# Kernel optimization log

Hardware: AMD Instinct MI355X
Metric: run time of the kernel (lower is better)

Reference implementation:

```python
import jax, jax.numpy as jnp
import numpy as np

EMBED_DIMS = 256

def setup_inputs() -> dict:
    key = jax.random.key(0)
    ks = jax.random.split(key, 6)
    C = EMBED_DIMS
    x = jax.random.normal(ks[0], (4, 2048, C), dtype=jnp.float32)
    prev_x = jax.random.normal(ks[1], (4, 2048, C), dtype=jnp.float32)
    s = 1.0 / np.sqrt(C)
    W_qkv = jax.random.uniform(ks[2], (C, 3 * C), dtype=jnp.float32, minval=-s, maxval=s)
    b_qkv = jax.random.uniform(ks[3], (3 * C,), dtype=jnp.float32, minval=-s, maxval=s)
    W_out = jax.random.uniform(ks[4], (C, C), dtype=jnp.float32, minval=-s, maxval=s)
    b_out = jax.random.uniform(ks[5], (C,), dtype=jnp.float32, minval=-s, maxval=s)
    return {"x": x, "prev_x": prev_x, "W_qkv": W_qkv, "b_qkv": b_qkv,
            "W_out": W_out, "b_out": b_out}

def reference(x, prev_x, W_qkv, b_qkv, W_out, b_out):
    B, N, C = x.shape
    xx = jnp.concatenate([prev_x, x], axis=1)          # [B, S, C], S = 2N
    qkv = xx @ W_qkv + b_qkv                            # [B, S, 3C]
    q, k, v = jnp.split(qkv, 3, axis=-1)                # each [B, S, C]
    scale = 1.0 / jnp.sqrt(jnp.asarray(C, dtype=x.dtype))
    attn = jax.nn.softmax(jnp.einsum('bqc,bkc->bqk', q, k) * scale, axis=-1)
    out = jnp.einsum('bqk,bkc->bqc', attn, v)           # [B, S, C]
    out = out @ W_out + b_out
    return out[:, -N:, :]                               # [B, N, C]
```

## Files before the change

### kernel.cpp

```cpp
#include <hip/hip_runtime.h>

typedef __bf16 bf16;
typedef __attribute__((ext_vector_type(8))) __bf16 bf16x8;
typedef __attribute__((ext_vector_type(4))) __bf16 bf16x4;
typedef __attribute__((ext_vector_type(4))) float f32x4;
typedef __attribute__((ext_vector_type(16))) float f32x16;
typedef __attribute__((ext_vector_type(4))) unsigned u32x4;

#define MFMA16(a, b, c) __builtin_amdgcn_mfma_f32_16x16x32_bf16(a, b, c, 0, 0, 0)
#define MFMA32(a, b, c) __builtin_amdgcn_mfma_f32_32x32x16_bf16(a, b, c, 0, 0, 0)

__device__ inline void gload_lds16(const void* g, void* l) {
  __builtin_amdgcn_global_load_lds(
      (const __attribute__((address_space(1))) void*)g,
      (__attribute__((address_space(3))) void*)l, 16, 0, 0);
}

__device__ inline unsigned packbf(float a, float b) {
  unsigned short x = __builtin_bit_cast(unsigned short, (bf16)a);
  unsigned short y = __builtin_bit_cast(unsigned short, (bf16)b);
  return (unsigned)x | ((unsigned)y << 16);
}

__global__ __launch_bounds__(256) void prep_w_kernel(
    const float* __restrict__ Wqkv, const float* __restrict__ Wout,
    bf16* __restrict__ Wqkvt, bf16* __restrict__ Woutt)
{
  int tid = blockIdx.x * 256 + threadIdx.x;
  int nth = gridDim.x * 256;
  for (int i = tid; i < 768 * 256; i += nth) {
    int n = i >> 8, k = i & 255;
    Wqkvt[i] = (bf16)Wqkv[k * 768 + n];
  }
  for (int i = tid; i < 256 * 256; i += nth) {
    int n = i >> 8, k = i & 255;
    Woutt[i] = (bf16)Wout[k * 256 + n];
  }
}

__global__ __launch_bounds__(256) void gemm_qkv_kernel(
    const float* __restrict__ x, const float* __restrict__ px,
    const bf16* __restrict__ Wt, const float* __restrict__ bias,
    bf16* __restrict__ Qo, bf16* __restrict__ KVo)
{
  const int bm = blockIdx.x * 64;
  const int n0 = blockIdx.y * 128;
  const int tid = threadIdx.x;
  const int lane = tid & 63, w = tid >> 6;
  const int l15 = lane & 15, lg = lane >> 4;

  alignas(16) __shared__ bf16 Alds[64 * 32];
  alignas(16) __shared__ bf16 Wlds[128 * 32];

  f32x4 acc[8] = {};

  for (int k0 = 0; k0 < 256; k0 += 32) {
    __syncthreads();
    {
      int c = tid;
      int row = c >> 2, kc = (c & 3) << 3;
      const int m = bm + row;
      const int b = m >> 12;
      const int s = m & 4095;
      const float* src = (s < 2048)
          ? (px + ((size_t)b << 19) + (size_t)s * 256 + k0 + kc)
          : (x + ((size_t)b << 19) + (size_t)(s - 2048) * 256 + k0 + kc);
      float4 f0 = *(const float4*)src;
      float4 f1 = *(const float4*)(src + 4);
      bf16x8 v = { (bf16)f0.x, (bf16)f0.y, (bf16)f0.z, (bf16)f0.w,
                   (bf16)f1.x, (bf16)f1.y, (bf16)f1.z, (bf16)f1.w };
      *(bf16x8*)((char*)Alds + ((c << 4) ^ (((row >> 1) & 3) << 4))) = v;
    }
    #pragma unroll
    for (int it = 0; it < 2; it++) {
      int c = it * 256 + tid;
      int row = c >> 2, kc = (c & 3) << 3;
      bf16x8 v = *(const bf16x8*)(Wt + (size_t)(n0 + row) * 256 + k0 + kc);
      *(bf16x8*)((char*)Wlds + ((c << 4) ^ (((row >> 1) & 3) << 4))) = v;
    }
    __syncthreads();
    const int arow = w * 16 + l15;
    bf16x8 afr = *(const bf16x8*)((char*)Alds +
        (((arow << 6) + (lg << 4)) ^ (((arow >> 1) & 3) << 4)));
    #pragma unroll
    for (int nt = 0; nt < 8; nt++) {
      const int wrow = nt * 16 + l15;
      bf16x8 bfr = *(const bf16x8*)((char*)Wlds +
          (((wrow << 6) + (lg << 4)) ^ (((wrow >> 1) & 3) << 4)));
      acc[nt] = MFMA16(afr, bfr, acc[nt]);
    }
  }

  #pragma unroll
  for (int nt = 0; nt < 8; nt++) {
    const int n = n0 + nt * 16 + l15;
    const float bv = bias[n];
    const int m0 = bm + w * 16 + lg * 4;
    const int bq = m0 >> 12;
    const int s = m0 & 4095;
    if (n < 256) {
      if (s >= 2048) {
        const int ks = n >> 4, h2 = (n >> 3) & 1, e = n & 7;
        #pragma unroll
        for (int r = 0; r < 4; r++) {
          const int qrow = bq * 2048 + (s - 2048) + r;
          Qo[(size_t)(qrow >> 5) * 8192 + ks * 512 +
             ((qrow & 31) + 32 * h2) * 8 + e] =
              (bf16)((acc[nt][r] + bv) * 0.0625f);
        }
      }
    } else if (n < 512) {
      const int d = n - 256;
      const int ks = d >> 4, h2 = (d >> 3) & 1, e = d & 7;
      const size_t tb = (size_t)(bq * 128 + (s >> 5)) * 16384;
      #pragma unroll
      for (int r = 0; r < 4; r++)
        KVo[tb + ks * 512 + (((s & 31) + r) + 32 * h2) * 8 + e] =
            (bf16)(acc[nt][r] + bv);
    } else {
      const int d = n - 512;
      const int kv32 = s & 31;
      const int sidx = kv32 >> 4, h2 = (kv32 >> 3) & 1, e0 = kv32 & 7;
      bf16x4 st = { (bf16)(acc[nt][0] + bv), (bf16)(acc[nt][1] + bv),
                    (bf16)(acc[nt][2] + bv), (bf16)(acc[nt][3] + bv) };
      *(bf16x4*)(KVo + (size_t)(bq * 128 + (s >> 5)) * 16384 + 8192 +
                 (sidx * 8 + (d >> 5)) * 512 + ((d & 31) + 32 * h2) * 8 + e0) = st;
    }
  }
}

__global__ __launch_bounds__(256, 2) void attn_kernel(
    const bf16* __restrict__ Qp, const bf16* __restrict__ KVp,
    bf16* __restrict__ Opart, float* __restrict__ ml)
{
  const int id = blockIdx.x;
  const int c = id & 7;
  const int b = (id >> 3) & 3;
  const int qb = id >> 5;
  const int tid = threadIdx.x;
  const int lane = tid & 63, w = tid >> 6;
  const int l31 = lane & 31, hi = lane >> 5;

  __shared__ bf16 lds[2][16384];

  const int qg = b * 64 + qb * 4 + w;
  const bf16* qbase = Qp + (size_t)qg * 8192 + lane * 8;
  bf16x8 qf[16];
  #pragma unroll
  for (int ks = 0; ks < 16; ks++)
    qf[ks] = *(const bf16x8*)(qbase + ks * 512);

  const bf16* kvtile0 = KVp + (size_t)(b * 128 + c * 16) * 16384;

  auto stage = [&](int t) {
    const char* g = (const char*)(kvtile0 + (size_t)t * 16384) + w * 8192 + lane * 16;
    char* l = (char*)&lds[t & 1][0] + w * 8192;
    #pragma unroll
    for (int j = 0; j < 8; j++)
      gload_lds16(g + j * 1024, l + j * 1024);
  };
  stage(0);

  f32x16 o[8] = {};
  float m_run = -1e30f, l_run = 0.f;

  for (int t = 0; t < 16; t++) {
    __syncthreads();
    if (t + 1 < 16) stage(t + 1);
    const bf16* kbuf = &lds[t & 1][0];
    const bf16* vbuf = kbuf + 8192;

    f32x16 p = {};
    __builtin_amdgcn_s_setprio(1);
    #pragma unroll
    for (int ks = 0; ks < 16; ks++) {
      bf16x8 kf = *(const bf16x8*)(kbuf + ks * 512 + lane * 8);
      p = MFMA32(kf, qf[ks], p);
    }
    __builtin_amdgcn_s_setprio(0);

    float mt = fmaxf(p[0], p[1]);
    #pragma unroll
    for (int i = 2; i < 16; i++) mt = fmaxf(mt, p[i]);
    mt = fmaxf(mt, __shfl_xor(mt, 32));
    if (!__all(mt <= m_run + 8.f)) {
      const float m_new = fmaxf(m_run, mt);
      const float alpha = __expf(m_run - m_new);
      l_run *= alpha;
      #pragma unroll
      for (int i = 0; i < 8; i++)
        #pragma unroll
        for (int j = 0; j < 16; j++) o[i][j] *= alpha;
      m_run = m_new;
    }
    float ps = 0.f;
    #pragma unroll
    for (int i = 0; i < 16; i++) { p[i] = __expf(p[i] - m_run); ps += p[i]; }
    ps += __shfl_xor(ps, 32);
    l_run += ps;

    unsigned u[8], xp[8];
    #pragma unroll
    for (int i = 0; i < 8; i++) u[i] = packbf(p[2 * i], p[2 * i + 1]);
    #pragma unroll
    for (int i = 0; i < 8; i++)
      xp[i] = (unsigned)__shfl_xor((int)u[i], 32);
    const u32x4 w0 = hi ? (u32x4){xp[2], xp[3], u[2], u[3]}
                        : (u32x4){u[0], u[1], xp[0], xp[1]};
    const u32x4 w1 = hi ? (u32x4){xp[6], xp[7], u[6], u[7]}
                        : (u32x4){u[4], u[5], xp[4], xp[5]};
    const bf16x8 pf0 = __builtin_bit_cast(bf16x8, w0);
    const bf16x8 pf1 = __builtin_bit_cast(bf16x8, w1);

    __builtin_amdgcn_s_setprio(1);
    #pragma unroll
    for (int dg = 0; dg < 8; dg++) {
      bf16x8 v0 = *(const bf16x8*)(vbuf + dg * 512 + lane * 8);
      o[dg] = MFMA32(v0, pf0, o[dg]);
      bf16x8 v1 = *(const bf16x8*)(vbuf + (8 + dg) * 512 + lane * 8);
      o[dg] = MFMA32(v1, pf1, o[dg]);
    }
    __builtin_amdgcn_s_setprio(0);
  }

  const int q = b * 2048 + qb * 128 + w * 32 + l31;
  bf16* ob = Opart + ((size_t)c * 8192 + q) * 256;
  #pragma unroll
  for (int dg = 0; dg < 8; dg++) {
    #pragma unroll
    for (int r4 = 0; r4 < 4; r4++) {
      const int d = dg * 32 + r4 * 8 + hi * 4;
      bf16x4 st = { (bf16)o[dg][r4 * 4 + 0], (bf16)o[dg][r4 * 4 + 1],
                    (bf16)o[dg][r4 * 4 + 2], (bf16)o[dg][r4 * 4 + 3] };
      *(bf16x4*)(ob + d) = st;
    }
  }
  if (hi == 0) {
    float2 v = { m_run, l_run };
    *(float2*)(ml + ((size_t)c * 8192 + q) * 2) = v;
  }
}

__global__ __launch_bounds__(256) void out_kernel(
    const bf16* __restrict__ Opart, const float* __restrict__ ml,
    const bf16* __restrict__ Woutt, const float* __restrict__ bout,
    float* __restrict__ out)
{
  const int bm = blockIdx.x * 32;
  const int tid = threadIdx.x;
  const int lane = tid & 63, w = tid >> 6;
  const int l15 = lane & 15, lg = lane >> 4;

  alignas(16) __shared__ bf16 Alds[32 * 256];
  alignas(16) __shared__ bf16 Wlds[256 * 32];

  #pragma unroll
  for (int ch = 0; ch < 4; ch++) {
    const int idx = ch * 256 + tid;
    const int row = idx >> 5;
    const int dc = (idx & 31) << 3;
    const int q = bm + row;
    float ms[8], ls[8], M = -1e30f;
    #pragma unroll
    for (int s = 0; s < 8; s++) {
      float2 v = *(const float2*)(ml + ((size_t)s * 8192 + q) * 2);
      ms[s] = v.x; ls[s] = v.y;
      M = fmaxf(M, v.x);
    }
    float L = 0.f, acc[8] = {};
    #pragma unroll
    for (int s = 0; s < 8; s++) {
      const float wgt = __expf(ms[s] - M);
      L += ls[s] * wgt;
      bf16x8 v = *(const bf16x8*)(Opart + ((size_t)s * 8192 + q) * 256 + dc);
      #pragma unroll
      for (int j = 0; j < 8; j++) acc[j] += wgt * (float)v[j];
    }
    const float inv = 1.f / L;
    bf16x8 st;
    #pragma unroll
    for (int j = 0; j < 8; j++) st[j] = (bf16)(acc[j] * inv);
    *(bf16x8*)((char*)Alds + ((row * 512 + dc * 2) ^ ((row & 7) << 4))) = st;
  }

  f32x4 acc[8] = {};
  for (int k0 = 0; k0 < 8; k0++) {
    __syncthreads();
    #pragma unroll
    for (int it = 0; it < 4; it++) {
      int cidx = it * 256 + tid;
      int row = cidx >> 2, kc = (cidx & 3) << 3;
      bf16x8 v = *(const bf16x8*)(Woutt + (size_t)row * 256 + k0 * 32 + kc);
      *(bf16x8*)((char*)Wlds + ((cidx << 4) ^ (((row >> 1) & 3) << 4))) = v;
    }
    __syncthreads();
    const int arow = (w & 1) * 16 + l15;
    bf16x8 afr = *(const bf16x8*)((char*)Alds +
        ((arow * 512 + k0 * 64 + lg * 16) ^ ((arow & 7) << 4)));
    #pragma unroll
    for (int nt = 0; nt < 8; nt++) {
      const int wrow = (w >> 1) * 128 + nt * 16 + l15;
      bf16x8 bfr = *(const bf16x8*)((char*)Wlds +
          (((wrow << 6) + (lg << 4)) ^ (((wrow >> 1) & 3) << 4)));
      acc[nt] = MFMA16(afr, bfr, acc[nt]);
    }
  }

  #pragma unroll
  for (int nt = 0; nt < 8; nt++) {
    const int n = (w >> 1) * 128 + nt * 16 + l15;
    const float bvv = bout[n];
    const int m0 = bm + (w & 1) * 16 + lg * 4;
    #pragma unroll
    for (int r = 0; r < 4; r++)
      out[(size_t)(m0 + r) * 256 + n] = acc[nt][r] + bvv;
  }
}

extern "C" void kernel_launch(void* const* d_in, const int* in_sizes, int n_in,
                              void* d_out, int out_size, void* d_ws, size_t ws_size,
                              hipStream_t stream) {
  const float* x    = (const float*)d_in[0];
  const float* px   = (const float*)d_in[1];
  const float* Wqkv = (const float*)d_in[2];
  const float* bqkv = (const float*)d_in[3];
  const float* Wout = (const float*)d_in[4];
  const float* bout = (const float*)d_in[5];
  float* out = (float*)d_out;

  char* ws = (char*)d_ws;
  bf16* Qp    = (bf16*)(ws);
  bf16* KVp   = (bf16*)(ws + 4194304);
  bf16* Woutt = (bf16*)(ws + 20971520);
  bf16* Wqkvt = (bf16*)(ws + 21102592);
  float* ml   = (float*)(ws + 21495808);
  bf16* Opart = (bf16*)(ws + 22020096);

  prep_w_kernel<<<dim3(128), dim3(256), 0, stream>>>(Wqkv, Wout, Wqkvt, Woutt);
  gemm_qkv_kernel<<<dim3(256, 6), dim3(256), 0, stream>>>(
      x, px, Wqkvt, bqkv, Qp, KVp);
  attn_kernel<<<dim3(512), dim3(256), 0, stream>>>(Qp, KVp, Opart, ml);
  out_kernel<<<dim3(256), dim3(256), 0, stream>>>(Opart, ml, Woutt, bout, out);
}
```

Baseline: 93.51 us.

## Skip unused Q projection for prev rows, widen QKV tiles, async-stage weights

The QKV GEMM moves to a 1D grid that leaves out the Q column blocks for prev_x rows, whose queries are discarded anyway, and doubles the M tile to 128 rows so each wave runs two MFMA row tiles. Weight tiles in both GEMMs are now loaded straight into LDS with global_load_lds, with the swizzle applied to the source address. The output projection double-buffers the weight tile, prefetching the next K slice while the current one computes, which drops one barrier per iteration. The costs are more accumulator registers and reliance on the barrier to complete the async LDS loads.

```diff
diff --git a/kernel.cpp b/kernel.cpp
--- a/kernel.cpp
+++ b/kernel.cpp
@@ -43,28 +43,34 @@
     const bf16* __restrict__ Wt, const float* __restrict__ bias,
     bf16* __restrict__ Qo, bf16* __restrict__ KVo)
 {
-  const int bm = blockIdx.x * 64;
-  const int n0 = blockIdx.y * 128;
+  const int idb = blockIdx.x;
+  const int b = idb / 160;
+  const int r = idb % 160;
+  int mblk, y;
+  if (r < 64) { mblk = r >> 2; y = 2 + (r & 3); }
+  else { int r2 = r - 64; mblk = 16 + r2 / 6; y = r2 % 6; }
+  const int bm = b * 4096 + mblk * 128;
+  const int n0 = y * 128;
+
   const int tid = threadIdx.x;
   const int lane = tid & 63, w = tid >> 6;
   const int l15 = lane & 15, lg = lane >> 4;
 
-  alignas(16) __shared__ bf16 Alds[64 * 32];
+  alignas(16) __shared__ bf16 Alds[128 * 32];
   alignas(16) __shared__ bf16 Wlds[128 * 32];
 
-  f32x4 acc[8] = {};
+  f32x4 acc[2][8] = {};
+
+  const float* xsrc = ((bm & 4095) < 2048) ? px : x;
+  const size_t xbase = ((size_t)b << 19) + (size_t)(bm & 2047) * 256;
 
   for (int k0 = 0; k0 < 256; k0 += 32) {
     __syncthreads();
-    {
-      int c = tid;
+    #pragma unroll
+    for (int it = 0; it < 2; it++) {
+      int c = it * 256 + tid;
       int row = c >> 2, kc = (c & 3) << 3;
-      const int m = bm + row;
-      const int b = m >> 12;
-      const int s = m & 4095;
-      const float* src = (s < 2048)
-          ? (px + ((size_t)b << 19) + (size_t)s * 256 + k0 + kc)
-          : (x + ((size_t)b << 19) + (size_t)(s - 2048) * 256 + k0 + kc);
+      const float* src = xsrc + xbase + (size_t)row * 256 + k0 + kc;
       float4 f0 = *(const float4*)src;
       float4 f1 = *(const float4*)(src + 4);
       bf16x8 v = { (bf16)f0.x, (bf16)f0.y, (bf16)f0.z, (bf16)f0.w,
@@ -72,59 +78,68 @@
       *(bf16x8*)((char*)Alds + ((c << 4) ^ (((row >> 1) & 3) << 4))) = v;
     }
     #pragma unroll
-    for (int it = 0; it < 2; it++) {
-      int c = it * 256 + tid;
-      int row = c >> 2, kc = (c & 3) << 3;
-      bf16x8 v = *(const bf16x8*)(Wt + (size_t)(n0 + row) * 256 + k0 + kc);
-      *(bf16x8*)((char*)Wlds + ((c << 4) ^ (((row >> 1) & 3) << 4))) = v;
+    for (int jj = 0; jj < 2; jj++) {
+      int j = w * 2 + jj;
+      int row = j * 16 + (lane >> 2);
+      int chunk = (lane & 3) ^ ((row >> 1) & 3);
+      const bf16* g = Wt + (size_t)(n0 + row) * 256 + k0 + chunk * 8;
+      gload_lds16(g, (char*)Wlds + j * 1024);
     }
     __syncthreads();
-    const int arow = w * 16 + l15;
-    bf16x8 afr = *(const bf16x8*)((char*)Alds +
-        (((arow << 6) + (lg << 4)) ^ (((arow >> 1) & 3) << 4)));
+
+    const int arow0 = w * 32 + l15;
+    bf16x8 af0 = *(const bf16x8*)((char*)Alds +
+        (((arow0 << 6) + (lg << 4)) ^ (((arow0 >> 1) & 3) << 4)));
+    const int arow1 = arow0 + 16;
+    bf16x8 af1 = *(const bf16x8*)((char*)Alds +
+        (((arow1 << 6) + (lg << 4)) ^ (((arow1 >> 1) & 3) << 4)));
     #pragma unroll
     for (int nt = 0; nt < 8; nt++) {
       const int wrow = nt * 16 + l15;
       bf16x8 bfr = *(const bf16x8*)((char*)Wlds +
           (((wrow << 6) + (lg << 4)) ^ (((wrow >> 1) & 3) << 4)));
-      acc[nt] = MFMA16(afr, bfr, acc[nt]);
-    }
-  }
-
-  #pragma unroll
-  for (int nt = 0; nt < 8; nt++) {
-    const int n = n0 + nt * 16 + l15;
-    const float bv = bias[n];
-    const int m0 = bm + w * 16 + lg * 4;
-    const int bq = m0 >> 12;
-    const int s = m0 & 4095;
-    if (n < 256) {
-      if (s >= 2048) {
-        const int ks = n >> 4, h2 = (n >> 3) & 1, e = n & 7;
+      acc[0][nt] = MFMA16(af0, bfr, acc[0][nt]);
+      acc[1][nt] = MFMA16(af1, bfr, acc[1][nt]);
+    }
+  }
+
+  #pragma unroll
+  for (int mt = 0; mt < 2; mt++) {
+    #pragma unroll
+    for (int nt = 0; nt < 8; nt++) {
+      const int n = n0 + nt * 16 + l15;
+      const float bv = bias[n];
+      const int m0 = bm + w * 32 + mt * 16 + lg * 4;
+      const int bq = m0 >> 12;
+      const int s = m0 & 4095;
+      if (n < 256) {
+        if (s >= 2048) {
+          const int ks = n >> 4, h2 = (n >> 3) & 1, e = n & 7;
+          #pragma unroll
+          for (int rr = 0; rr < 4; rr++) {
+            const int qrow = bq * 2048 + (s - 2048) + rr;
+            Qo[(size_t)(qrow >> 5) * 8192 + ks * 512 +
+               ((qrow & 31) + 32 * h2) * 8 + e] =
+                (bf16)((acc[mt][nt][rr] + bv) * 0.0625f);
+          }
+        }
+      } else if (n < 512) {
+        const int d = n - 256;
+        const int ks = d >> 4, h2 = (d >> 3) & 1, e = d & 7;
+        const size_t tb = (size_t)(bq * 128 + (s >> 5)) * 16384;
         #pragma unroll
-        for (int r = 0; r < 4; r++) {
-          const int qrow = bq * 2048 + (s - 2048) + r;
-          Qo[(size_t)(qrow >> 5) * 8192 + ks * 512 +
-             ((qrow & 31) + 32 * h2) * 8 + e] =
-              (bf16)((acc[nt][r] + bv) * 0.0625f);
-        }
+        for (int rr = 0; rr < 4; rr++)
+          KVo[tb + ks * 512 + (((s & 31) + rr) + 32 * h2) * 8 + e] =
+              (bf16)(acc[mt][nt][rr] + bv);
+      } else {
+        const int d = n - 512;
+        const int kv32 = s & 31;
+        const int sidx = kv32 >> 4, h2 = (kv32 >> 3) & 1, e0 = kv32 & 7;
+        bf16x4 st = { (bf16)(acc[mt][nt][0] + bv), (bf16)(acc[mt][nt][1] + bv),
+                      (bf16)(acc[mt][nt][2] + bv), (bf16)(acc[mt][nt][3] + bv) };
+        *(bf16x4*)(KVo + (size_t)(bq * 128 + (s >> 5)) * 16384 + 8192 +
+                   (sidx * 8 + (d >> 5)) * 512 + ((d & 31) + 32 * h2) * 8 + e0) = st;
       }
-    } else if (n < 512) {
-      const int d = n - 256;
-      const int ks = d >> 4, h2 = (d >> 3) & 1, e = d & 7;
-      const size_t tb = (size_t)(bq * 128 + (s >> 5)) * 16384;
-      #pragma unroll
-      for (int r = 0; r < 4; r++)
-        KVo[tb + ks * 512 + (((s & 31) + r) + 32 * h2) * 8 + e] =
-            (bf16)(acc[nt][r] + bv);
-    } else {
-      const int d = n - 512;
-      const int kv32 = s & 31;
-      const int sidx = kv32 >> 4, h2 = (kv32 >> 3) & 1, e0 = kv32 & 7;
-      bf16x4 st = { (bf16)(acc[nt][0] + bv), (bf16)(acc[nt][1] + bv),
-                    (bf16)(acc[nt][2] + bv), (bf16)(acc[nt][3] + bv) };
-      *(bf16x4*)(KVo + (size_t)(bq * 128 + (s >> 5)) * 16384 + 8192 +
-                 (sidx * 8 + (d >> 5)) * 512 + ((d & 31) + 32 * h2) * 8 + e0) = st;
     }
   }
 }
@@ -252,7 +267,19 @@
   const int l15 = lane & 15, lg = lane >> 4;
 
   alignas(16) __shared__ bf16 Alds[32 * 256];
-  alignas(16) __shared__ bf16 Wlds[256 * 32];
+  alignas(16) __shared__ bf16 Wlds[2][256 * 32];
+
+  auto stageW = [&](int k0) {
+    #pragma unroll
+    for (int jj = 0; jj < 4; jj++) {
+      int j = w * 4 + jj;
+      int row = j * 16 + (lane >> 2);
+      int chunk = (lane & 3) ^ ((row >> 1) & 3);
+      const bf16* g = Woutt + (size_t)row * 256 + k0 * 32 + chunk * 8;
+      gload_lds16(g, (char*)&Wlds[k0 & 1][0] + j * 1024);
+    }
+  };
+  stageW(0);
 
   #pragma unroll
   for (int ch = 0; ch < 4; ch++) {
@@ -282,28 +309,23 @@
     for (int j = 0; j < 8; j++) st[j] = (bf16)(acc[j] * inv);
     *(bf16x8*)((char*)Alds + ((row * 512 + dc * 2) ^ ((row & 7) << 4))) = st;
   }
+  __syncthreads();
 
   f32x4 acc[8] = {};
   for (int k0 = 0; k0 < 8; k0++) {
-    __syncthreads();
-    #pragma unroll
-    for (int it = 0; it < 4; it++) {
-      int cidx = it * 256 + tid;
-      int row = cidx >> 2, kc = (cidx & 3) << 3;
-      bf16x8 v = *(const bf16x8*)(Woutt + (size_t)row * 256 + k0 * 32 + kc);
-      *(bf16x8*)((char*)Wlds + ((cidx << 4) ^ (((row >> 1) & 3) << 4))) = v;
-    }
-    __syncthreads();
+    if (k0 + 1 < 8) stageW(k0 + 1);
+    const bf16* wbuf = &Wlds[k0 & 1][0];
     const int arow = (w & 1) * 16 + l15;
     bf16x8 afr = *(const bf16x8*)((char*)Alds +
         ((arow * 512 + k0 * 64 + lg * 16) ^ ((arow & 7) << 4)));
     #pragma unroll
     for (int nt = 0; nt < 8; nt++) {
       const int wrow = (w >> 1) * 128 + nt * 16 + l15;
-      bf16x8 bfr = *(const bf16x8*)((char*)Wlds +
+      bf16x8 bfr = *(const bf16x8*)((char*)wbuf +
           (((wrow << 6) + (lg << 4)) ^ (((wrow >> 1) & 3) << 4)));
       acc[nt] = MFMA16(afr, bfr, acc[nt]);
     }
+    __syncthreads();
   }
 
   #pragma unroll
@@ -337,7 +359,7 @@
   bf16* Opart = (bf16*)(ws + 22020096);
 
   prep_w_kernel<<<dim3(128), dim3(256), 0, stream>>>(Wqkv, Wout, Wqkvt, Woutt);
-  gemm_qkv_kernel<<<dim3(256, 6), dim3(256), 0, stream>>>(
+  gemm_qkv_kernel<<<dim3(640), dim3(256), 0, stream>>>(
       x, px, Wqkvt, bqkv, Qp, KVp);
   attn_kernel<<<dim3(512), dim3(256), 0, stream>>>(Qp, KVp, Opart, ml);
   out_kernel<<<dim3(256), dim3(256), 0, stream>>>(Opart, ml, Woutt, bout, out);
```

New measurement: 91.05 us. 2.6% less time.
